# Kernel optimization log

Measured on AMD Instinct MI355X. Metric: run time of the kernel, lower is better.

## Reference

```python
import jax, jax.numpy as jnp
import numpy as np

B, S, E, H, VS, VT = 128, 256, 512, 512, 32000, 32000


def _lstm_layer(x, mask, Wih, Whh, bih, bhh):
    # x: (S,B,E_in), mask: (S,B) bool. PyTorch gate order i,f,g,o.
    h0 = jnp.zeros((x.shape[1], Whh.shape[1]), x.dtype)
    c0 = h0
    def step(carry, inp):
        h, c = carry
        xt, mt = inp
        g = xt @ Wih.T + h @ Whh.T + bih + bhh
        i, f, gg, o = jnp.split(g, 4, axis=-1)
        i = jax.nn.sigmoid(i); f = jax.nn.sigmoid(f)
        gg = jnp.tanh(gg); o = jax.nn.sigmoid(o)
        c_new = f * c + i * gg
        h_new = o * jnp.tanh(c_new)
        m = mt[:, None]
        h2 = jnp.where(m, h_new, h)
        c2 = jnp.where(m, c_new, c)
        return (h2, c2), jnp.where(m, h_new, 0.0)  # pad_packed zero-pads
    (hT, cT), ys = jax.lax.scan(step, (h0, c0), (x, mask))
    return ys, cT


def setup_inputs() -> dict:
    key = jax.random.key(0)
    ks = jax.random.split(key, 32)
    def w(k, shape, fan_in):
        bound = 1.0 / np.sqrt(fan_in)
        return jax.random.uniform(k, shape, jnp.float32, -bound, bound)
    src_tokens = jax.random.randint(ks[0], (B, S), 0, VS)
    src_lens = jnp.sort(jax.random.randint(ks[1], (B,), S // 2, S + 1))[::-1]
    src_lens = src_lens.at[0].set(S)  # pack_padded expects descending, max = S
    trg_tokens = jax.random.randint(ks[2], (B,), 0, VT)
    inp = {
        'src_tokens': src_tokens, 'src_lens': src_lens, 'trg_tokens': trg_tokens,
        'src_emb': jax.random.normal(ks[3], (VS, E), jnp.float32),
        'trg_emb': jax.random.normal(ks[4], (VT, E), jnp.float32),
        'enc_Wih0': w(ks[5], (4 * H, E), H), 'enc_Whh0': w(ks[6], (4 * H, H), H),
        'enc_bih0': w(ks[7], (4 * H,), H), 'enc_bhh0': w(ks[8], (4 * H,), H),
        'enc_Wih1': w(ks[9], (4 * H, H), H), 'enc_Whh1': w(ks[10], (4 * H, H), H),
        'enc_bih1': w(ks[11], (4 * H,), H), 'enc_bhh1': w(ks[12], (4 * H,), H),
        'dec_Wih': w(ks[13], (4 * H, E + H), H), 'dec_Whh': w(ks[14], (4 * H, H), H),
        'dec_bih': w(ks[15], (4 * H,), H), 'dec_bhh': w(ks[16], (4 * H,), H),
        'W_init': w(ks[17], (H, 2 * H), 2 * H), 'b_init': w(ks[18], (H,), 2 * H),
        'W_hid': w(ks[19], (H, 2 * H), 2 * H), 'b_hid': w(ks[20], (H,), 2 * H),
        'W_out': w(ks[21], (VT, H), H), 'b_out': w(ks[22], (VT,), H),
    }
    return inp


def reference(src_tokens, src_lens, trg_tokens, src_emb, trg_emb,
              enc_Wih0, enc_Whh0, enc_bih0, enc_bhh0,
              enc_Wih1, enc_Whh1, enc_bih1, enc_bhh1,
              dec_Wih, dec_Whh, dec_bih, dec_bhh,
              W_init, b_init, W_hid, b_hid, W_out, b_out):
    # ---- encode ----
    x = src_emb[src_tokens]                       # (B,S,E)
    x = jnp.transpose(x, (1, 0, 2))               # (S,B,E)
    mask = jnp.arange(S)[:, None] < src_lens[None, :]  # (S,B)
    y0, c0f = _lstm_layer(x, mask, enc_Wih0, enc_Whh0, enc_bih0, enc_bhh0)
    y1, c1f = _lstm_layer(y0, mask, enc_Wih1, enc_Whh1, enc_bih1, enc_bhh1)
    src_states = jnp.transpose(y1, (1, 0, 2))     # (B,S,H)
    # final cell states (num_layers,B,H) -> (B, num_layers*H)
    final_cells = jnp.concatenate([c0f, c1f], axis=-1)  # (B,2H)
    c_dec = final_cells @ W_init.T + b_init       # (B,H)
    h_dec = jnp.tanh(c_dec)
    # ---- one decoder step ----
    emb_t = trg_emb[trg_tokens]                   # (B,E)
    vec = jnp.concatenate([emb_t, jnp.zeros((B, H), emb_t.dtype)], axis=-1)
    g = vec @ dec_Wih.T + h_dec @ dec_Whh.T + dec_bih + dec_bhh
    i, f, gg, o = jnp.split(g, 4, axis=-1)
    c = jax.nn.sigmoid(f) * c_dec + jax.nn.sigmoid(i) * jnp.tanh(gg)
    h = jax.nn.sigmoid(o) * jnp.tanh(c)           # (B,H)
    # ---- masked dot attention ----
    scores = jnp.einsum('bsh,bh->bs', src_states, h)
    smask = jnp.arange(S)[None, :] < src_lens[:, None]
    scores = jnp.where(smask, scores, -jnp.inf)
    attw = jax.nn.softmax(scores, axis=-1)
    context = jnp.einsum('bs,bsh->bh', attw, src_states)
    attn_vec = jnp.concatenate([h, context], axis=-1) @ W_hid.T + b_hid
    logits = attn_vec @ W_out.T + b_out
    prd_token = jnp.argmax(logits, axis=-1)       # softmax is monotone
    return context, h, prd_token
```

## Files before the change

kernel.cpp:

```cpp
#include <hip/hip_runtime.h>
#include <stdint.h>


typedef _Float16 f16;
typedef f16 f16x8 __attribute__((ext_vector_type(8)));
typedef float f32x4 __attribute__((ext_vector_type(4)));

#define LOSCALE 2048.0f
#define LOINV   (1.0f/2048.0f)

#define B_  128
#define S_  256
#define H_  512

__device__ __forceinline__ uint16_t hbits(f16 h){ union{ f16 f; uint16_t u; } c; c.f=h; return c.u; }

__device__ __forceinline__ uint32_t split_ph2(float x){
  f16 h = (f16)x;
  float r = (x - (float)h) * LOSCALE;
  return (uint32_t)hbits(h) | ((uint32_t)hbits((f16)r) << 16);
}
__device__ __forceinline__ float ph2val(uint32_t p){
  union{ uint16_t u; f16 f; } a, b; a.u = (uint16_t)p; b.u = (uint16_t)(p>>16);
  return (float)a.f + (float)b.f * LOINV;
}

__device__ __forceinline__ void pack_hi_lo(const uint4& a, const uint4& b, uint4& hi, uint4& lo){
  hi = make_uint4((a.x & 0xffffu) | (a.y << 16),
                  (a.z & 0xffffu) | (a.w << 16),
                  (b.x & 0xffffu) | (b.y << 16),
                  (b.z & 0xffffu) | (b.w << 16));
  lo = make_uint4((a.x >> 16) | (a.y & 0xffff0000u),
                  (a.z >> 16) | (a.w & 0xffff0000u),
                  (b.x >> 16) | (b.y & 0xffff0000u),
                  (b.z >> 16) | (b.w & 0xffff0000u));
}

__device__ __forceinline__ void split_pack8(const float* x, uint4& hi, uint4& lo){
  uint16_t h[8], l[8];
#pragma unroll
  for (int e = 0; e < 8; ++e) {
    f16 hh = (f16)x[e];
    float r = (x[e] - (float)hh) * LOSCALE;
    h[e] = hbits(hh); l[e] = hbits((f16)r);
  }
  hi = make_uint4((uint32_t)h[0]|((uint32_t)h[1]<<16), (uint32_t)h[2]|((uint32_t)h[3]<<16),
                  (uint32_t)h[4]|((uint32_t)h[5]<<16), (uint32_t)h[6]|((uint32_t)h[7]<<16));
  lo = make_uint4((uint32_t)l[0]|((uint32_t)l[1]<<16), (uint32_t)l[2]|((uint32_t)l[3]<<16),
                  (uint32_t)l[4]|((uint32_t)l[5]<<16), (uint32_t)l[6]|((uint32_t)l[7]<<16));
}

__device__ __forceinline__ f32x4 mfma16(uint4 a, uint4 b, f32x4 c){
  return __builtin_amdgcn_mfma_f32_16x16x32_f16(
      __builtin_bit_cast(f16x8, a), __builtin_bit_cast(f16x8, b), c, 0, 0, 0);
}

__device__ __forceinline__ float sigm(float x){ return 1.0f/(1.0f + expf(-x)); }
__device__ __forceinline__ float fsigm(float x){ return 1.0f/(1.0f + __expf(-x)); }
__device__ __forceinline__ float ftanh(float x){
  float ax = fabsf(x);
  float e = __expf(-2.0f*ax);
  float r = (1.0f - e)/(1.0f + e);
  return copysignf(r, x);
}

__device__ __forceinline__ uint32_t plane_word(uint32_t p, uint32_t pp, int odd){
  return odd ? ((pp >> 16) | (p & 0xffff0000u))
             : ((p & 0xffffu) | (pp << 16));
}

__device__ __forceinline__ size_t fl_idx(int row, int k){
  return (size_t)(k >> 5) * 4096 + (size_t)(row >> 4) * 512 + (size_t)(k & 1) * 256
       + (size_t)((k >> 3) & 3) * 64 + (size_t)(row & 15) * 4 + (size_t)((k & 7) >> 1);
}

__device__ __forceinline__ void gload_lds16(const uint32_t* gbase, uint32_t* lbase, int lane){
#if __has_builtin(__builtin_amdgcn_global_load_lds)
  __builtin_amdgcn_global_load_lds(
      (const __attribute__((address_space(1))) uint32_t*)(gbase + lane*4),
      (__attribute__((address_space(3))) uint32_t*)lbase, 16, 0, 0);
#else
  *(uint4*)(lbase + lane*4) = *(const uint4*)(gbase + lane*4);
#endif
}

__global__ __launch_bounds__(256) void k_embed_src_fl(const int* __restrict__ tok,
    const float* __restrict__ emb, uint32_t* __restrict__ out)
{
  const size_t total = (size_t)S_ * B_ * H_;
  for (size_t i = (size_t)blockIdx.x*256 + threadIdx.x; i < total; i += (size_t)gridDim.x*256) {
    int s = (int)(i >> 16), b = (int)((i >> 9) & 127), k = (int)(i & 511);
    int t = tok[b*S_ + s];
    uint32_t p = split_ph2(emb[(size_t)t*H_ + k]);
    uint32_t pp = __shfl_xor(p, 1);
    out[(size_t)s*65536 + fl_idx(b, k)] = plane_word(p, pp, k & 1);
  }
}

__global__ __launch_bounds__(256) void k_embed_trg(const int* __restrict__ tok,
    const float* __restrict__ emb, uint32_t* __restrict__ out)
{
  int i = blockIdx.x*256 + threadIdx.x;
  int e = i & (H_-1), b = i >> 9;
  int t = tok[b];
  out[i] = split_ph2(emb[(size_t)t*H_ + e]);
}

__global__ __launch_bounds__(256) void k_packW(const float* __restrict__ W,
    uint32_t* __restrict__ out)
{
  int i = blockIdx.x*256 + threadIdx.x;
  int n = i >> 9, k = i & 511;
  uint32_t p = split_ph2(W[i]);
  uint32_t pp = __shfl_xor(p, 1);
  out[(size_t)(n >> 7)*65536 + fl_idx(n & 127, k)] = plane_word(p, pp, k & 1);
}

__global__ __launch_bounds__(256) void k_packAfl(const float* __restrict__ a,
    uint32_t* __restrict__ out)
{
  int i = blockIdx.x*256 + threadIdx.x;
  int b = i >> 9, k = i & 511;
  uint32_t p = split_ph2(a[i]);
  uint32_t pp = __shfl_xor(p, 1);
  out[fl_idx(b, k)] = plane_word(p, pp, k & 1);
}

__global__ __launch_bounds__(256,2) void k_gemm_fl(
    const uint32_t* __restrict__ Afl,
    const uint32_t* __restrict__ Wfl,
    const float* __restrict__ b0, const float* __restrict__ b1,
    float* __restrict__ C, int N, int addC)
{
  __shared__ uint8_t sm[65536];
  const int tid = threadIdx.x, lane = tid & 63, wv = tid >> 6;
  const int wm = wv >> 1, wn = wv & 1;
  const int bn0 = blockIdx.x * 128, bm0 = blockIdx.y * 128;
  const uint32_t* Ab = Afl + (size_t)blockIdx.y * 65536;
  const uint32_t* Wb = Wfl + (size_t)blockIdx.x * 65536;

  f32x4 acc0[4][4], acc1[4][4];
#pragma unroll
  for (int i = 0; i < 4; ++i)
#pragma unroll
    for (int j = 0; j < 4; ++j) { acc0[i][j] = (f32x4){0,0,0,0}; acc1[i][j] = (f32x4){0,0,0,0}; }

  for (int it = 0; it < 8; ++it) {
    __syncthreads();
    {
      const uint32_t* gsrc = (wv < 2 ? Ab : Wb) + (size_t)it*8192 + (size_t)(wv & 1)*4096;
      uint32_t* lb = (uint32_t*)(sm + (size_t)wv*16384);
#pragma unroll
      for (int e = 0; e < 16; ++e)
        gload_lds16(gsrc + e*256, lb + e*256, lane);
    }
    asm volatile("s_waitcnt vmcnt(0)" ::: "memory");
    __syncthreads();

#pragma unroll
    for (int kt = 0; kt < 2; ++kt) {
      uint4 ah[4], al[4];
#pragma unroll
      for (int i = 0; i < 4; ++i) {
        const uint8_t* p = sm + (size_t)(kt*8 + wm*4 + i)*2048 + lane*16;
        ah[i] = *(const uint4*)p; al[i] = *(const uint4*)(p + 1024);
      }
#pragma unroll
      for (int j = 0; j < 4; ++j) {
        const uint8_t* p = sm + 32768 + (size_t)(kt*8 + wn*4 + j)*2048 + lane*16;
        uint4 bh = *(const uint4*)p;
        uint4 bl = *(const uint4*)(p + 1024);
#pragma unroll
        for (int i = 0; i < 4; ++i) {
          acc0[i][j] = mfma16(ah[i], bh, acc0[i][j]);
          acc1[i][j] = mfma16(al[i], bh, acc1[i][j]);
          acc1[i][j] = mfma16(ah[i], bl, acc1[i][j]);
        }
      }
    }
  }

#pragma unroll
  for (int i = 0; i < 4; ++i) {
    int row0 = bm0 + (wm*4+i)*16 + ((lane>>4)<<2);
#pragma unroll
    for (int j = 0; j < 4; ++j) {
      int col = bn0 + (wn*4+j)*16 + (lane & 15);
      float bias = 0.f;
      if (b0) bias += b0[col];
      if (b1) bias += b1[col];
      f32x4 v = acc0[i][j] + acc1[i][j] * LOINV;
#pragma unroll
      for (int r = 0; r < 4; ++r) {
        size_t idx = (size_t)(row0 + r) * N + col;
        float out = v[r] + bias;
        if (addC) out += C[idx];
        C[idx] = out;
      }
    }
  }
}

__global__ __launch_bounds__(256,2) void k_gemm(
    const uint32_t* __restrict__ A, int lda,
    const float* __restrict__ W, int ldw,
    const float* __restrict__ b0, const float* __restrict__ b1,
    float* __restrict__ C, int N, int K, int addC)
{
  __shared__ uint8_t sm[65536];
  const int tid = threadIdx.x;
  const int lane = tid & 63, wv = tid >> 6;
  const int wm = wv >> 1, wn = wv & 1;
  const int bn0 = blockIdx.x * 128, bm0 = blockIdx.y * 128;

  const int srow = tid >> 1;
  const int skh  = (tid & 1) * 32;
  const int smt  = srow >> 4, sr = srow & 15, skt = tid & 1;

  f32x4 acc0[4][4], acc1[4][4];
#pragma unroll
  for (int i = 0; i < 4; ++i)
#pragma unroll
    for (int j = 0; j < 4; ++j) { acc0[i][j] = (f32x4){0,0,0,0}; acc1[i][j] = (f32x4){0,0,0,0}; }

  for (int k0 = 0; k0 < K; k0 += 64) {
    __syncthreads();
    {
      const uint32_t* ap = A + (size_t)(bm0 + srow) * lda + (k0 + skh);
      uint4 q[8];
#pragma unroll
      for (int e = 0; e < 8; ++e) q[e] = *(const uint4*)(ap + e*4);
#pragma unroll
      for (int kg = 0; kg < 4; ++kg) {
        uint4 hi, lo; pack_hi_lo(q[2*kg], q[2*kg+1], hi, lo);
        uint8_t* dst = sm + (size_t)(smt*2 + skt)*2048 + (size_t)(sr + 16*kg)*16;
        *(uint4*)dst = hi; *(uint4*)(dst + 1024) = lo;
      }
    }
    {
      const float* wp = W + (size_t)(bn0 + srow) * ldw + (k0 + skh);
      float xs[32];
#pragma unroll
      for (int e = 0; e < 8; ++e) { float4 v = *(const float4*)(wp + e*4);
        xs[e*4+0]=v.x; xs[e*4+1]=v.y; xs[e*4+2]=v.z; xs[e*4+3]=v.w; }
#pragma unroll
      for (int kg = 0; kg < 4; ++kg) {
        uint4 hi, lo; split_pack8(xs + kg*8, hi, lo);
        uint8_t* dst = sm + 32768 + (size_t)(smt*2 + skt)*2048 + (size_t)(sr + 16*kg)*16;
        *(uint4*)dst = hi; *(uint4*)(dst + 1024) = lo;
      }
    }
    __syncthreads();

#pragma unroll
    for (int kt = 0; kt < 2; ++kt) {
      uint4 ah[4], al[4];
#pragma unroll
      for (int i = 0; i < 4; ++i) {
        const uint8_t* p = sm + (size_t)(((wm*4+i)*2 + kt))*2048 + lane*16;
        ah[i] = *(const uint4*)p; al[i] = *(const uint4*)(p + 1024);
      }
#pragma unroll
      for (int j = 0; j < 4; ++j) {
        const uint8_t* p = sm + 32768 + (size_t)(((wn*4+j)*2 + kt))*2048 + lane*16;
        uint4 bh = *(const uint4*)p;
        uint4 bl = *(const uint4*)(p + 1024);
#pragma unroll
        for (int i = 0; i < 4; ++i) {
          acc0[i][j] = mfma16(ah[i], bh, acc0[i][j]);
          acc1[i][j] = mfma16(al[i], bh, acc1[i][j]);
          acc1[i][j] = mfma16(ah[i], bl, acc1[i][j]);
        }
      }
    }
  }

#pragma unroll
  for (int i = 0; i < 4; ++i) {
    int row0 = bm0 + (wm*4+i)*16 + ((lane>>4)<<2);
#pragma unroll
    for (int j = 0; j < 4; ++j) {
      int col = bn0 + (wn*4+j)*16 + (lane & 15);
      float bias = 0.f;
      if (b0) bias += b0[col];
      if (b1) bias += b1[col];
      f32x4 v = acc0[i][j] + acc1[i][j] * LOINV;
#pragma unroll
      for (int r = 0; r < 4; ++r) {
        size_t idx = (size_t)(row0 + r) * N + col;
        float out = v[r] + bias;
        if (addC) out += C[idx];
        C[idx] = out;
      }
    }
  }
}

__global__ __launch_bounds__(256,1) void k_lstm(
    const float* __restrict__ Whh,
    const float* __restrict__ xg,
    const int*  __restrict__ lens,
    uint32_t* __restrict__ hbuf,
    float* __restrict__ cbuf,
    uint32_t* __restrict__ ybuf,
    uint32_t* __restrict__ flags,
    int s0, int nsteps)
{
  __shared__ uint64_t htile64[4096];
  __shared__ float gates_lds[1024];
  uint8_t* htile = (uint8_t*)htile64;
  const int tid = threadIdx.x, lane = tid & 63, wv = tid >> 6;
  const int bg = blockIdx.x & 7, hs = blockIdx.x >> 3;
  const int row = lane & 15, qh = lane >> 4;

  uint4 wbh[16], wbl[16];
  {
    const float* wrow = Whh + (size_t)(wv*512 + hs*16 + row) * 512 + qh*8;
#pragma unroll
    for (int kt = 0; kt < 16; ++kt) {
      float xs[8];
      float4 v0 = *(const float4*)(wrow + kt*32);
      float4 v1 = *(const float4*)(wrow + kt*32 + 4);
      xs[0]=v0.x; xs[1]=v0.y; xs[2]=v0.z; xs[3]=v0.w;
      xs[4]=v1.x; xs[5]=v1.y; xs[6]=v1.z; xs[7]=v1.w;
      split_pack8(xs, wbh[kt], wbl[kt]);
    }
  }

  const int b_l = tid >> 4, uu = tid & 15;
  const int bglob = bg*16 + b_l;
  const size_t bgoff = (size_t)bg*8192;
  const int oct_p = hs*2 + (uu >> 3);
  const size_t widx = (size_t)b_l*512 + (size_t)(uu & 1)*256
                    + (size_t)((oct_p ^ b_l) << 2) + (size_t)((uu & 7) >> 1);
  float c_reg = cbuf[(size_t)bglob*512 + hs*16 + uu];
  float h_reg;
  {
    size_t ib = (size_t)(s0 & 1)*65536 + bgoff + (size_t)b_l*512
              + (size_t)((oct_p ^ b_l) << 2) + (size_t)((uu & 7) >> 1);
    uint32_t hiw = hbuf[ib];
    uint32_t low = hbuf[ib + 256];
    int sh = (uu & 1) * 16;
    union{ uint16_t u; f16 f; } ch, cl;
    ch.u = (uint16_t)(hiw >> sh); cl.u = (uint16_t)(low >> sh);
    h_reg = (float)ch.f + (float)cl.f * LOINV;
  }
  const int len_b = lens[bglob];
  const size_t yfl = (size_t)(hs >> 1)*4096 + (size_t)bg*512 + (size_t)(uu & 1)*256
                   + (size_t)((((hs & 1) << 1) | (uu >> 3)))*64 + (size_t)b_l*4
                   + (size_t)((uu & 7) >> 1);
  int sidx[8];
#pragma unroll
  for (int e = 0; e < 8; ++e) {
    int j = e*256 + tid; int r2 = j >> 7, sub = j & 127;
    sidx[e] = r2*256 + ((sub >> 6) << 7) + (sub & 63);
  }
  __syncthreads();

  for (int sl = 0; sl < nsteps; ++sl) {
    const int s = s0 + sl;

    const float* xgp = xg + ((size_t)sl*128 + bglob)*2048 + hs*16 + uu;
    float xv0 = xgp[0], xv1 = xgp[512], xv2 = xgp[1024], xv3 = xgp[1536];

    if (sl > 0) {
      if (wv == 0) {
        const uint32_t* fp = flags + bg*32 + (lane & 31);
        while (1) {
          uint32_t f = __hip_atomic_load(fp, __ATOMIC_RELAXED, __HIP_MEMORY_SCOPE_SYSTEM);
          if (__all((int)(f >= (uint32_t)s))) break;
          __builtin_amdgcn_s_sleep(1);
        }
      }
      __syncthreads();
    }

    const uint64_t* src = (const uint64_t*)(hbuf + (size_t)(s & 1)*65536 + bgoff);
    uint64_t v0[8], v1[8];
#pragma unroll
    for (int e = 0; e < 8; ++e)
      v0[e] = __hip_atomic_load(src + sidx[e], __ATOMIC_RELAXED, __HIP_MEMORY_SCOPE_SYSTEM);
#pragma unroll
    for (int e = 0; e < 8; ++e)
      v1[e] = __hip_atomic_load(src + sidx[e] + 64, __ATOMIC_RELAXED, __HIP_MEMORY_SCOPE_SYSTEM);
#pragma unroll
    for (int e = 0; e < 8; ++e)
      htile64[sidx[e]] = v0[e];
    asm volatile("s_waitcnt lgkmcnt(0)" ::: "memory");
    __builtin_amdgcn_s_barrier();
    __builtin_amdgcn_sched_barrier(0);

    f32x4 a0 = (f32x4){0,0,0,0}, a1 = (f32x4){0,0,0,0}, a2 = (f32x4){0,0,0,0};
    const uint8_t* hrowp = htile + (size_t)row*2048;
#pragma unroll
    for (int kt = 0; kt < 8; ++kt) {
      int oct = kt*4 + qh;
      const uint8_t* p = hrowp + (((oct ^ row)) << 4);
      uint4 ah = *(const uint4*)p;
      uint4 al = *(const uint4*)(p + 1024);
      a0 = mfma16(ah, wbh[kt], a0);
      a1 = mfma16(al, wbh[kt], a1);
      a2 = mfma16(ah, wbl[kt], a2);
    }
#pragma unroll
    for (int e = 0; e < 8; ++e)
      htile64[sidx[e] + 64] = v1[e];
    asm volatile("s_waitcnt lgkmcnt(0)" ::: "memory");
    __builtin_amdgcn_s_barrier();
    __builtin_amdgcn_sched_barrier(0);
#pragma unroll
    for (int kt = 8; kt < 16; ++kt) {
      int oct = kt*4 + qh;
      const uint8_t* p = hrowp + (((oct ^ row)) << 4);
      uint4 ah = *(const uint4*)p;
      uint4 al = *(const uint4*)(p + 1024);
      a0 = mfma16(ah, wbh[kt], a0);
      a1 = mfma16(al, wbh[kt], a1);
      a2 = mfma16(ah, wbl[kt], a2);
    }
    {
      int col = lane & 15, rbase = (lane >> 4) << 2;
#pragma unroll
      for (int r = 0; r < 4; ++r)
        gates_lds[(size_t)(wv*16 + rbase + r)*16 + col] = a0[r] + (a1[r] + a2[r])*LOINV;
    }
    __syncthreads();

    float gi = gates_lds[(size_t)(0*16 + b_l)*16 + uu] + xv0;
    float gf = gates_lds[(size_t)(1*16 + b_l)*16 + uu] + xv1;
    float gg = gates_lds[(size_t)(2*16 + b_l)*16 + uu] + xv2;
    float go = gates_lds[(size_t)(3*16 + b_l)*16 + uu] + xv3;
    float cn = fsigm(gf)*c_reg + fsigm(gi)*ftanh(gg);
    float hn = fsigm(go)*ftanh(cn);
    bool m = (s < len_b);
    c_reg = m ? cn : c_reg;
    h_reg = m ? hn : h_reg;

    uint32_t p = split_ph2(h_reg);
    uint32_t pp = __shfl_xor(p, 1);
    uint32_t wword = plane_word(p, pp, uu & 1);
    __hip_atomic_store(hbuf + (size_t)((s + 1) & 1)*65536 + bgoff + widx,
                       wword, __ATOMIC_RELAXED, __HIP_MEMORY_SCOPE_SYSTEM);
    asm volatile("s_waitcnt vmcnt(0)" ::: "memory");
    __syncthreads();
    if (tid == 0)
      __hip_atomic_store(flags + bg*32 + hs, (uint32_t)(s + 1),
                         __ATOMIC_RELAXED, __HIP_MEMORY_SCOPE_SYSTEM);
    ybuf[(size_t)s*65536 + yfl] = m ? wword : 0u;
  }
  cbuf[(size_t)bglob*512 + hs*16 + uu] = c_reg;
}

__global__ __launch_bounds__(256) void k_pack2(const float* __restrict__ a,
    const float* __restrict__ b, uint32_t* __restrict__ out)
{
  int i = blockIdx.x*256 + threadIdx.x;
  int bb = i >> 10, k = i & 1023;
  float x = (k < 512) ? a[(size_t)bb*512 + k] : b[(size_t)bb*512 + k - 512];
  out[i] = split_ph2(x);
}

__global__ __launch_bounds__(256) void k_tanh_split(const float* __restrict__ c,
    uint32_t* __restrict__ hp)
{ int i = blockIdx.x*256 + threadIdx.x; hp[i] = split_ph2(tanhf(c[i])); }

__global__ __launch_bounds__(256) void k_dec_cell(const float* __restrict__ g,
    const float* __restrict__ cdec, float* __restrict__ hout, float* __restrict__ dh)
{
  int i = blockIdx.x*256 + threadIdx.x;
  int b = i >> 9, u = i & 511;
  const float* gb = g + (size_t)b*2048;
  float c = sigm(gb[512 + u])*cdec[i] + sigm(gb[u])*tanhf(gb[1024 + u]);
  float h = sigm(gb[1536 + u])*tanhf(c);
  hout[i] = h; dh[i] = h;
}

__global__ __launch_bounds__(256) void k_attn(const uint32_t* __restrict__ y1,
    const float* __restrict__ h, const int* __restrict__ lens,
    float* __restrict__ ctx, float* __restrict__ dctx)
{
  __shared__ float hsh[512];
  __shared__ float sc[256];
  __shared__ float red[8];
  const int b = blockIdx.x, tid = threadIdx.x, lane = tid & 63, wv = tid >> 6;
  hsh[tid]       = h[(size_t)b*512 + tid];
  hsh[tid + 256] = h[(size_t)b*512 + tid + 256];
  const int len = lens[b];
  __syncthreads();

  const size_t lanebase = (size_t)(lane >> 2)*4096 + (size_t)(b >> 4)*512
                        + (size_t)(lane & 3)*64 + (size_t)(b & 15)*4;
  for (int it = 0; it < 64; ++it) {
    int s = wv*64 + it;
    const uint32_t* yb = y1 + (size_t)s*65536 + lanebase;
    uint4 hw = *(const uint4*)yb;
    uint4 lw = *(const uint4*)(yb + 256);
    int k0 = lane*8;
    uint32_t hws[4] = {hw.x,hw.y,hw.z,hw.w}, lws[4] = {lw.x,lw.y,lw.z,lw.w};
    float d = 0.f;
#pragma unroll
    for (int w = 0; w < 4; ++w) {
      union{uint16_t u; f16 f;} h0,h1,l0,l1;
      h0.u=(uint16_t)hws[w]; h1.u=(uint16_t)(hws[w]>>16);
      l0.u=(uint16_t)lws[w]; l1.u=(uint16_t)(lws[w]>>16);
      d += ((float)h0.f + (float)l0.f*LOINV) * hsh[k0 + 2*w]
         + ((float)h1.f + (float)l1.f*LOINV) * hsh[k0 + 2*w + 1];
    }
    for (int off = 32; off; off >>= 1) d += __shfl_xor(d, off);
    if (lane == 0) sc[s] = d;
  }
  __syncthreads();

  float v = (tid < len) ? sc[tid] : -INFINITY;
  float mx = v;
  for (int off = 32; off; off >>= 1) mx = fmaxf(mx, __shfl_xor(mx, off));
  if (lane == 0) red[wv] = mx;
  __syncthreads();
  mx = fmaxf(fmaxf(red[0], red[1]), fmaxf(red[2], red[3]));
  float e = (tid < len) ? expf(v - mx) : 0.f;
  float ssum = e;
  for (int off = 32; off; off >>= 1) ssum += __shfl_xor(ssum, off);
  if (lane == 0) red[4 + wv] = ssum;
  __syncthreads();
  float tot = red[4] + red[5] + red[6] + red[7];
  __syncthreads();
  sc[tid] = e / tot;
  __syncthreads();

  const int u0 = tid, u1 = tid + 256;
  const size_t bu0 = (size_t)(u0 >> 5)*4096 + (size_t)(b >> 4)*512
                   + (size_t)((u0 >> 3) & 3)*64 + (size_t)(b & 15)*4 + (size_t)((u0 & 7) >> 1);
  const size_t bu1 = (size_t)(u1 >> 5)*4096 + (size_t)(b >> 4)*512
                   + (size_t)((u1 >> 3) & 3)*64 + (size_t)(b & 15)*4 + (size_t)((u1 & 7) >> 1);
  const int sh = (tid & 1) * 16;
  float acc0 = 0.f, acc1 = 0.f;
  for (int s = 0; s < 256; ++s) {
    float w = sc[s];
    const uint32_t* yb = y1 + (size_t)s*65536;
    uint32_t hi0 = yb[bu0], lo0 = yb[bu0 + 256];
    uint32_t hi1 = yb[bu1], lo1 = yb[bu1 + 256];
    union{uint16_t u; f16 f;} a,b2,c2,d2;
    a.u =(uint16_t)(hi0 >> sh); b2.u=(uint16_t)(lo0 >> sh);
    c2.u=(uint16_t)(hi1 >> sh); d2.u=(uint16_t)(lo1 >> sh);
    acc0 += w*((float)a.f  + (float)b2.f*LOINV);
    acc1 += w*((float)c2.f + (float)d2.f*LOINV);
  }
  ctx [(size_t)b*512 + tid]       = acc0;  ctx [(size_t)b*512 + tid + 256] = acc1;
  dctx[(size_t)b*512 + tid]       = acc0;  dctx[(size_t)b*512 + tid + 256] = acc1;
}

__global__ __launch_bounds__(256) void k_argmax(const float* __restrict__ logits,
    float* __restrict__ out)
{
  __shared__ float bv[256];
  __shared__ int   bi[256];
  const int b = blockIdx.x, tid = threadIdx.x;
  const float* L = logits + (size_t)b*32000;
  float best = -INFINITY; int idx = 0;
  for (int i = tid; i < 32000; i += 256) {
    float v = L[i];
    if (v > best) { best = v; idx = i; }
  }
  bv[tid] = best; bi[tid] = idx;
  __syncthreads();
  for (int sft = 128; sft; sft >>= 1) {
    if (tid < sft) {
      if (bv[tid+sft] > bv[tid] || (bv[tid+sft] == bv[tid] && bi[tid+sft] < bi[tid])) {
        bv[tid] = bv[tid+sft]; bi[tid] = bi[tid+sft];
      }
    }
    __syncthreads();
  }
  if (tid == 0) out[b] = (float)bi[0];
}

extern "C" void kernel_launch(void* const* d_in, const int* in_sizes, int n_in,
                              void* d_out, int out_size, void* d_ws, size_t ws_size,
                              hipStream_t stream)
{
  (void)in_sizes; (void)n_in; (void)out_size; (void)ws_size;
  const int*   src_tokens = (const int*)  d_in[0];
  const int*   src_lens   = (const int*)  d_in[1];
  const int*   trg_tokens = (const int*)  d_in[2];
  const float* src_emb    = (const float*)d_in[3];
  const float* trg_emb    = (const float*)d_in[4];
  const float* Wih0 = (const float*)d_in[5];
  const float* Whh0 = (const float*)d_in[6];
  const float* bih0 = (const float*)d_in[7];
  const float* bhh0 = (const float*)d_in[8];
  const float* Wih1 = (const float*)d_in[9];
  const float* Whh1 = (const float*)d_in[10];
  const float* bih1 = (const float*)d_in[11];
  const float* bhh1 = (const float*)d_in[12];
  const float* dWih = (const float*)d_in[13];
  const float* dWhh = (const float*)d_in[14];
  const float* dbih = (const float*)d_in[15];
  const float* dbhh = (const float*)d_in[16];
  const float* Winit= (const float*)d_in[17];
  const float* binit= (const float*)d_in[18];
  const float* Whid = (const float*)d_in[19];
  const float* bhid = (const float*)d_in[20];
  const float* Wout = (const float*)d_in[21];
  const float* bout = (const float*)d_in[22];

  uint8_t* ws = (uint8_t*)d_ws;
  constexpr size_t MBs = 1ull << 20;
  constexpr size_t OFF_AP    = 0;
  constexpr size_t OFF_Y0    = 64*MBs;
  constexpr size_t OFF_XG    = 128*MBs;
  constexpr size_t OFF_HBUF  = 192*MBs;
  constexpr size_t OFF_CB0   = OFF_HBUF  + 512*1024;
  constexpr size_t OFF_CB1   = OFF_CB0   + 256*1024;
  constexpr size_t OFF_FLG   = OFF_CB1   + 256*1024;
  constexpr size_t OFF_PK    = OFF_FLG   + 4096;
  constexpr size_t OFF_CDEC  = OFF_PK    + 512*1024;
  constexpr size_t OFF_HDECP = OFF_CDEC  + 256*1024;
  constexpr size_t OFF_EMBP  = OFF_HDECP + 256*1024;
  constexpr size_t OFF_G     = OFF_EMBP  + 256*1024;
  constexpr size_t OFF_HDEC2 = OFF_G     + 1*MBs;
  constexpr size_t OFF_CTX   = OFF_HDEC2 + 256*1024;
  constexpr size_t OFF_AVEC  = OFF_CTX   + 256*1024;
  constexpr size_t OFF_AVECP = OFF_AVEC  + 256*1024;
  constexpr size_t OFF_LOG   = OFF_AVECP + 256*1024;

  uint32_t* Ap    = (uint32_t*)(ws + OFF_AP);
  uint32_t* Y0    = (uint32_t*)(ws + OFF_Y0);
  uint32_t* Y1    = (uint32_t*)(ws + OFF_AP);
  float*    Xg    = (float*)   (ws + OFF_XG);
  uint32_t* WoutF = (uint32_t*)(ws + OFF_XG);
  uint32_t* hbuf  = (uint32_t*)(ws + OFF_HBUF);
  float*    cb0   = (float*)   (ws + OFF_CB0);
  float*    cb1   = (float*)   (ws + OFF_CB1);
  uint32_t* flg   = (uint32_t*)(ws + OFF_FLG);
  uint32_t* pk    = (uint32_t*)(ws + OFF_PK);
  float*    cdec  = (float*)   (ws + OFF_CDEC);
  uint32_t* hdecp = (uint32_t*)(ws + OFF_HDECP);
  uint32_t* embp  = (uint32_t*)(ws + OFF_EMBP);
  float*    g     = (float*)   (ws + OFF_G);
  float*    hdec2 = (float*)   (ws + OFF_HDEC2);
  float*    ctx   = (float*)   (ws + OFF_CTX);
  float*    avec  = (float*)   (ws + OFF_AVEC);
  uint32_t* avecp = (uint32_t*)(ws + OFF_AVECP);
  float*    logit = (float*)   (ws + OFF_LOG);
  uint32_t* Wp0   = (uint32_t*)(ws + OFF_LOG);
  uint32_t* Wp1   = (uint32_t*)(ws + OFF_LOG + 4*MBs);
  float*    dout  = (float*)   d_out;

  k_packW<<<4096, 256, 0, stream>>>(Wih0, Wp0);
  k_packW<<<4096, 256, 0, stream>>>(Wih1, Wp1);

  hipMemsetAsync(flg,  0, 1024, stream);
  hipMemsetAsync(hbuf, 0, 2*65536*4, stream);
  hipMemsetAsync(cb0,  0, 65536*4, stream);
  k_embed_src_fl<<<2048, 256, 0, stream>>>(src_tokens, src_emb, Ap);
  for (int c = 0; c < 4; ++c) {
    int s0 = c * 64;
    k_gemm_fl<<<dim3(16, 64), 256, 0, stream>>>(Ap + (size_t)s0*65536,
        Wp0, bih0, bhh0, Xg, 2048, 0);
    k_lstm<<<256, 256, 0, stream>>>(Whh0, Xg, src_lens, hbuf, cb0, Y0, flg, s0, 64);
  }
  hipMemsetAsync(flg,  0, 1024, stream);
  hipMemsetAsync(hbuf, 0, 2*65536*4, stream);
  hipMemsetAsync(cb1,  0, 65536*4, stream);
  for (int c = 0; c < 4; ++c) {
    int s0 = c * 64;
    k_gemm_fl<<<dim3(16, 64), 256, 0, stream>>>(Y0 + (size_t)s0*65536,
        Wp1, bih1, bhh1, Xg, 2048, 0);
    k_lstm<<<256, 256, 0, stream>>>(Whh1, Xg, src_lens, hbuf, cb1, Y1, flg, s0, 64);
  }

  k_packW<<<64000, 256, 0, stream>>>(Wout, WoutF);

  k_pack2<<<512, 256, 0, stream>>>(cb0, cb1, pk);
  k_gemm<<<dim3(4, 1), 256, 0, stream>>>(pk, 1024, Winit, 1024, binit, nullptr,
      cdec, 512, 1024, 0);
  k_tanh_split<<<256, 256, 0, stream>>>(cdec, hdecp);

  k_embed_trg<<<256, 256, 0, stream>>>(trg_tokens, trg_emb, embp);
  k_gemm<<<dim3(16, 1), 256, 0, stream>>>(embp, 512, dWih, 1024, dbih, dbhh,
      g, 2048, 512, 0);
  k_gemm<<<dim3(16, 1), 256, 0, stream>>>(hdecp, 512, dWhh, 512, nullptr, nullptr,
      g, 2048, 512, 1);
  k_dec_cell<<<256, 256, 0, stream>>>(g, cdec, hdec2, dout + 65536);

  k_attn<<<128, 256, 0, stream>>>(Y1, hdec2, src_lens, ctx, dout);

  k_pack2<<<512, 256, 0, stream>>>(hdec2, ctx, pk);
  k_gemm<<<dim3(4, 1), 256, 0, stream>>>(pk, 1024, Whid, 1024, bhid, nullptr,
      avec, 512, 1024, 0);
  k_packAfl<<<256, 256, 0, stream>>>(avec, avecp);
  k_gemm_fl<<<dim3(250, 1), 256, 0, stream>>>(avecp, WoutF, bout, nullptr,
      logit, 32000, 0);
  k_argmax<<<128, 256, 0, stream>>>(logit, dout + 131072);
}
```

Before: 2.775 ms.

## Replace flag-based LSTM step sync with tagged 64-bit hidden-state words

The persistent LSTM kernel no longer publishes per-block step flags after draining its stores with a barrier. Each hidden-state word is now a 64-bit store holding the hi and lo f16 planes, with a two-bit step parity tag packed into the low bits of the lo plane. Consumers poll the words directly and retry only those whose tag does not match. This removes the store-wait, barrier and flag round trip on every recurrent step, and the h-tile load is no longer split into two LDS phases. In exchange it gives up two mantissa bits of the lo residual and relies on 64-bit atomic stores being seen whole.

```diff
diff --git a/kernel.cpp b/kernel.cpp
--- a/kernel.cpp
+++ b/kernel.cpp
@@ -300,15 +300,13 @@
     const float* __restrict__ Whh,
     const float* __restrict__ xg,
     const int*  __restrict__ lens,
-    uint32_t* __restrict__ hbuf,
+    uint64_t* __restrict__ hbuf,
     float* __restrict__ cbuf,
     uint32_t* __restrict__ ybuf,
-    uint32_t* __restrict__ flags,
     int s0, int nsteps)
 {
-  __shared__ uint64_t htile64[4096];
+  __shared__ uint32_t htile[8192];
   __shared__ float gates_lds[1024];
-  uint8_t* htile = (uint8_t*)htile64;
   const int tid = threadIdx.x, lane = tid & 63, wv = tid >> 6;
   const int bg = blockIdx.x & 7, hs = blockIdx.x >> 3;
   const int row = lane & 15, qh = lane >> 4;
@@ -329,17 +327,13 @@
 
   const int b_l = tid >> 4, uu = tid & 15;
   const int bglob = bg*16 + b_l;
-  const size_t bgoff = (size_t)bg*8192;
-  const int oct_p = hs*2 + (uu >> 3);
-  const size_t widx = (size_t)b_l*512 + (size_t)(uu & 1)*256
-                    + (size_t)((oct_p ^ b_l) << 2) + (size_t)((uu & 7) >> 1);
+  const size_t bgq = (size_t)bg*4096;
+  const size_t wq  = (size_t)b_l*256 + hs*8 + (uu>>1);
   float c_reg = cbuf[(size_t)bglob*512 + hs*16 + uu];
   float h_reg;
   {
-    size_t ib = (size_t)(s0 & 1)*65536 + bgoff + (size_t)b_l*512
-              + (size_t)((oct_p ^ b_l) << 2) + (size_t)((uu & 7) >> 1);
-    uint32_t hiw = hbuf[ib];
-    uint32_t low = hbuf[ib + 256];
+    uint64_t q0 = hbuf[(size_t)(s0 & 1)*32768 + bgq + wq];
+    uint32_t hiw = (uint32_t)q0, low = (uint32_t)(q0 >> 32);
     int sh = (uu & 1) * 16;
     union{ uint16_t u; f16 f; } ch, cl;
     ch.u = (uint16_t)(hiw >> sh); cl.u = (uint16_t)(low >> sh);
@@ -349,12 +343,7 @@
   const size_t yfl = (size_t)(hs >> 1)*4096 + (size_t)bg*512 + (size_t)(uu & 1)*256
                    + (size_t)((((hs & 1) << 1) | (uu >> 3)))*64 + (size_t)b_l*4
                    + (size_t)((uu & 7) >> 1);
-  int sidx[8];
-#pragma unroll
-  for (int e = 0; e < 8; ++e) {
-    int j = e*256 + tid; int r2 = j >> 7, sub = j & 127;
-    sidx[e] = r2*256 + ((sub >> 6) << 7) + (sub & 63);
-  }
+  const int soct = tid >> 2, sword = tid & 3;
   __syncthreads();
 
   for (int sl = 0; sl < nsteps; ++sl) {
@@ -363,57 +352,51 @@
     const float* xgp = xg + ((size_t)sl*128 + bglob)*2048 + hs*16 + uu;
     float xv0 = xgp[0], xv1 = xgp[512], xv2 = xgp[1024], xv3 = xgp[1536];
 
-    if (sl > 0) {
-      if (wv == 0) {
-        const uint32_t* fp = flags + bg*32 + (lane & 31);
-        while (1) {
-          uint32_t f = __hip_atomic_load(fp, __ATOMIC_RELAXED, __HIP_MEMORY_SCOPE_SYSTEM);
-          if (__all((int)(f >= (uint32_t)s))) break;
-          __builtin_amdgcn_s_sleep(1);
-        }
-      }
-      __syncthreads();
-    }
-
-    const uint64_t* src = (const uint64_t*)(hbuf + (size_t)(s & 1)*65536 + bgoff);
-    uint64_t v0[8], v1[8];
-#pragma unroll
-    for (int e = 0; e < 8; ++e)
-      v0[e] = __hip_atomic_load(src + sidx[e], __ATOMIC_RELAXED, __HIP_MEMORY_SCOPE_SYSTEM);
-#pragma unroll
-    for (int e = 0; e < 8; ++e)
-      v1[e] = __hip_atomic_load(src + sidx[e] + 64, __ATOMIC_RELAXED, __HIP_MEMORY_SCOPE_SYSTEM);
-#pragma unroll
-    for (int e = 0; e < 8; ++e)
-      htile64[sidx[e]] = v0[e];
-    asm volatile("s_waitcnt lgkmcnt(0)" ::: "memory");
-    __builtin_amdgcn_s_barrier();
-    __builtin_amdgcn_sched_barrier(0);
+    const uint64_t* src = hbuf + (size_t)(s & 1)*32768 + bgq;
+    const uint32_t want = (uint32_t)(s & 1) | ((uint32_t)((s >> 1) & 1) << 16);
+    uint64_t v[16];
+    uint32_t pend;
+    {
+#pragma unroll
+      for (int e = 0; e < 16; ++e)
+        v[e] = __hip_atomic_load(src + e*256 + tid, __ATOMIC_RELAXED,
+                                 __HIP_MEMORY_SCOPE_SYSTEM);
+      uint32_t np = 0;
+#pragma unroll
+      for (int e = 0; e < 16; ++e)
+        if ((((uint32_t)(v[e] >> 32)) & 0x00010001u) != want) np |= 1u << e;
+      pend = np;
+    }
+    while (!__all((int)(pend == 0))) {
+      __builtin_amdgcn_s_sleep(2);
+#pragma unroll
+      for (int e = 0; e < 16; ++e)
+        if (pend & (1u << e))
+          v[e] = __hip_atomic_load(src + e*256 + tid, __ATOMIC_RELAXED,
+                                   __HIP_MEMORY_SCOPE_SYSTEM);
+      uint32_t np = 0;
+#pragma unroll
+      for (int e = 0; e < 16; ++e)
+        if ((pend & (1u << e)) &&
+            (((uint32_t)(v[e] >> 32)) & 0x00010001u) != want) np |= 1u << e;
+      pend = np;
+    }
+#pragma unroll
+    for (int e = 0; e < 16; ++e) {
+      int base = e*512 + ((soct ^ e) << 2) + sword;
+      htile[base]       = (uint32_t)v[e];
+      htile[base + 256] = (uint32_t)(v[e] >> 32);
+    }
+    __syncthreads();
 
     f32x4 a0 = (f32x4){0,0,0,0}, a1 = (f32x4){0,0,0,0}, a2 = (f32x4){0,0,0,0};
-    const uint8_t* hrowp = htile + (size_t)row*2048;
-#pragma unroll
-    for (int kt = 0; kt < 8; ++kt) {
+    const uint32_t* hrowp = htile + (size_t)row*512;
+#pragma unroll
+    for (int kt = 0; kt < 16; ++kt) {
       int oct = kt*4 + qh;
-      const uint8_t* p = hrowp + (((oct ^ row)) << 4);
+      const uint32_t* p = hrowp + ((oct ^ row) << 2);
       uint4 ah = *(const uint4*)p;
-      uint4 al = *(const uint4*)(p + 1024);
-      a0 = mfma16(ah, wbh[kt], a0);
-      a1 = mfma16(al, wbh[kt], a1);
-      a2 = mfma16(ah, wbl[kt], a2);
-    }
-#pragma unroll
-    for (int e = 0; e < 8; ++e)
-      htile64[sidx[e] + 64] = v1[e];
-    asm volatile("s_waitcnt lgkmcnt(0)" ::: "memory");
-    __builtin_amdgcn_s_barrier();
-    __builtin_amdgcn_sched_barrier(0);
-#pragma unroll
-    for (int kt = 8; kt < 16; ++kt) {
-      int oct = kt*4 + qh;
-      const uint8_t* p = hrowp + (((oct ^ row)) << 4);
-      uint4 ah = *(const uint4*)p;
-      uint4 al = *(const uint4*)(p + 1024);
+      uint4 al = *(const uint4*)(p + 256);
       a0 = mfma16(ah, wbh[kt], a0);
       a1 = mfma16(al, wbh[kt], a1);
       a2 = mfma16(ah, wbl[kt], a2);
@@ -438,14 +421,16 @@
 
     uint32_t p = split_ph2(h_reg);
     uint32_t pp = __shfl_xor(p, 1);
+    if (!(uu & 1)) {
+      uint32_t hi_w = (p & 0xffffu) | (pp << 16);
+      uint32_t lo_w = (p >> 16) | (pp & 0xffff0000u);
+      uint32_t ntag = (uint32_t)((s + 1) & 1) | ((uint32_t)(((s + 1) >> 1) & 1) << 16);
+      lo_w = (lo_w & 0xFFFEFFFEu) | ntag;
+      uint64_t qv = (uint64_t)hi_w | ((uint64_t)lo_w << 32);
+      __hip_atomic_store(hbuf + (size_t)((s + 1) & 1)*32768 + bgq + wq, qv,
+                         __ATOMIC_RELAXED, __HIP_MEMORY_SCOPE_SYSTEM);
+    }
     uint32_t wword = plane_word(p, pp, uu & 1);
-    __hip_atomic_store(hbuf + (size_t)((s + 1) & 1)*65536 + bgoff + widx,
-                       wword, __ATOMIC_RELAXED, __HIP_MEMORY_SCOPE_SYSTEM);
-    asm volatile("s_waitcnt vmcnt(0)" ::: "memory");
-    __syncthreads();
-    if (tid == 0)
-      __hip_atomic_store(flags + bg*32 + hs, (uint32_t)(s + 1),
-                         __ATOMIC_RELAXED, __HIP_MEMORY_SCOPE_SYSTEM);
     ybuf[(size_t)s*65536 + yfl] = m ? wword : 0u;
   }
   cbuf[(size_t)bglob*512 + hs*16 + uu] = c_reg;
@@ -609,10 +594,9 @@
   constexpr size_t OFF_Y0    = 64*MBs;
   constexpr size_t OFF_XG    = 128*MBs;
   constexpr size_t OFF_HBUF  = 192*MBs;
-  constexpr size_t OFF_CB0   = OFF_HBUF  + 512*1024;
+  constexpr size_t OFF_CB0   = OFF_HBUF  + 1*MBs;
   constexpr size_t OFF_CB1   = OFF_CB0   + 256*1024;
-  constexpr size_t OFF_FLG   = OFF_CB1   + 256*1024;
-  constexpr size_t OFF_PK    = OFF_FLG   + 4096;
+  constexpr size_t OFF_PK    = OFF_CB1   + 256*1024;
   constexpr size_t OFF_CDEC  = OFF_PK    + 512*1024;
   constexpr size_t OFF_HDECP = OFF_CDEC  + 256*1024;
   constexpr size_t OFF_EMBP  = OFF_HDECP + 256*1024;
@@ -628,10 +612,9 @@
   uint32_t* Y1    = (uint32_t*)(ws + OFF_AP);
   float*    Xg    = (float*)   (ws + OFF_XG);
   uint32_t* WoutF = (uint32_t*)(ws + OFF_XG);
-  uint32_t* hbuf  = (uint32_t*)(ws + OFF_HBUF);
+  uint64_t* hbuf  = (uint64_t*)(ws + OFF_HBUF);
   float*    cb0   = (float*)   (ws + OFF_CB0);
   float*    cb1   = (float*)   (ws + OFF_CB1);
-  uint32_t* flg   = (uint32_t*)(ws + OFF_FLG);
   uint32_t* pk    = (uint32_t*)(ws + OFF_PK);
   float*    cdec  = (float*)   (ws + OFF_CDEC);
   uint32_t* hdecp = (uint32_t*)(ws + OFF_HDECP);
@@ -649,24 +632,22 @@
   k_packW<<<4096, 256, 0, stream>>>(Wih0, Wp0);
   k_packW<<<4096, 256, 0, stream>>>(Wih1, Wp1);
 
-  hipMemsetAsync(flg,  0, 1024, stream);
-  hipMemsetAsync(hbuf, 0, 2*65536*4, stream);
+  hipMemsetAsync(hbuf, 0, 2*32768*8, stream);
   hipMemsetAsync(cb0,  0, 65536*4, stream);
   k_embed_src_fl<<<2048, 256, 0, stream>>>(src_tokens, src_emb, Ap);
   for (int c = 0; c < 4; ++c) {
     int s0 = c * 64;
     k_gemm_fl<<<dim3(16, 64), 256, 0, stream>>>(Ap + (size_t)s0*65536,
         Wp0, bih0, bhh0, Xg, 2048, 0);
-    k_lstm<<<256, 256, 0, stream>>>(Whh0, Xg, src_lens, hbuf, cb0, Y0, flg, s0, 64);
-  }
-  hipMemsetAsync(flg,  0, 1024, stream);
-  hipMemsetAsync(hbuf, 0, 2*65536*4, stream);
+    k_lstm<<<256, 256, 0, stream>>>(Whh0, Xg, src_lens, hbuf, cb0, Y0, s0, 64);
+  }
+  hipMemsetAsync(hbuf, 0, 2*32768*8, stream);
   hipMemsetAsync(cb1,  0, 65536*4, stream);
   for (int c = 0; c < 4; ++c) {
     int s0 = c * 64;
     k_gemm_fl<<<dim3(16, 64), 256, 0, stream>>>(Y0 + (size_t)s0*65536,
         Wp1, bih1, bhh1, Xg, 2048, 0);
-    k_lstm<<<256, 256, 0, stream>>>(Whh1, Xg, src_lens, hbuf, cb1, Y1, flg, s0, 64);
+    k_lstm<<<256, 256, 0, stream>>>(Whh1, Xg, src_lens, hbuf, cb1, Y1, s0, 64);
   }
 
   k_packW<<<64000, 256, 0, stream>>>(Wout, WoutF);
```

New measurement: 3.183 ms. 1.15x slower.
